# Optimization experiments

Hardware: AMD Instinct MI355X
Metric: run time of the kernel (lower is better)

## Reference

```python
import jax, jax.numpy as jnp
import numpy as np

GRID = 4096
WINDOW_SIZES = (128, 256, 512)  # self.window_schedule in the torch module
BLOCK_FRAC = 0.2                # fraction of blocked (fixed) cells


def setup_inputs() -> dict:
    key = jax.random.key(0)
    u = jax.random.uniform(key, (GRID, GRID), dtype=jnp.float32)
    # blocked cells > 0.0, free cells == 0.0 (binary fixed-cell occupancy mask)
    mask = (u > (1.0 - BLOCK_FRAC)).astype(jnp.float32)
    # the torch code requires the grid center (or an 8-neighbor) to be free;
    # force it free so the seed location is static.
    mask = mask.at[GRID // 2, GRID // 2].set(0.0)
    return {"fixed_cell_mask": mask}


def _dilate4(r):
    # 4-connected dilation of a boolean map (matches BFS neighbor set)
    up = jnp.pad(r[1:, :], ((0, 1), (0, 0)))
    dn = jnp.pad(r[:-1, :], ((1, 0), (0, 0)))
    lf = jnp.pad(r[:, 1:], ((0, 0), (0, 1)))
    rt = jnp.pad(r[:, :-1], ((0, 0), (1, 0)))
    return r | up | dn | lf | rt


def _flood_fill(free, cx, cy):
    """Parallel label-propagation equivalent of the serial BFS flood fill:
    reachable set of `free` cells 4-connected to seed (cx, cy). The seed is
    always tagged, exactly as in get_contiguous_free_region_in_window."""
    seed = jnp.zeros(free.shape, dtype=bool).at[cx, cy].set(True)

    def cond(state):
        reach, prev_count = state
        return jnp.sum(reach) != prev_count

    def body(state):
        reach, _ = state
        new = (_dilate4(reach) & free) | seed
        return new, jnp.sum(reach)

    reach, _ = jax.lax.while_loop(cond, body, (seed, jnp.int32(-1)))
    return reach


def reference(fixed_cell_mask):
    """Faithful JAX version of assemble_free_region_masks: for each window
    size, extract the centered window, flood-fill the contiguous free region
    from the center, and scatter it back into a full-grid boolean mask.
    Returns (masks [len(WINDOW_SIZES), H, W] float32, counts [len] int32)."""
    H, W = fixed_cell_mask.shape
    cx, cy = H // 2, W // 2  # seed is free by construction (see setup_inputs)
    masks, counts = [], []
    for size in WINDOW_SIZES:
        half = size // 2
        sx, ex = max(0, cx - half), min(H, cx + half)
        sy, ey = max(0, cy - half), min(W, cy + half)
        window = fixed_cell_mask[sx:ex, sy:ey]
        free = window == 0.0
        reach = _flood_fill(free, cx - sx, cy - sy)
        full = jnp.zeros((H, W), dtype=bool).at[sx:ex, sy:ey].set(reach)
        masks.append(full)
        counts.append(jnp.sum(reach))
    return jnp.stack(masks).astype(jnp.float32), jnp.stack(counts).astype(jnp.int32)
```

## Files before the change

kernel.cpp:

```cpp
#include <hip/hip_runtime.h>
#include <stdint.h>

#define GRID_N 4096
#define CCL_BLOCKS 336
#define ZERO_BLOCKS 8192
#define K1_BLOCKS (CCL_BLOCKS + ZERO_BLOCKS)
#define CELL_BLOCKS 1344
#define NUM_EDGES 19712
#define EDGE_BLOCKS 77

typedef float vfloat4 __attribute__((ext_vector_type(4)));

__device__ inline void decode_block(int b, int& w, int& S, int& lg, int& off,
                                    int& woff, int& baseblk) {
    if (b < 64)       { w = 0; S = 128; lg = 7; off = 1984; woff = 0;     baseblk = 0;   }
    else if (b < 320) { w = 1; S = 256; lg = 8; off = 1920; woff = 16384; baseblk = 64;  }
    else              { w = 2; S = 512; lg = 9; off = 1792; woff = 81920; baseblk = 320; }
}

__device__ inline void decode_tile(int b, int& S, int& lg, int& off, int& woff,
                                   int& tileR, int& tileC) {
    int t, tsh;
    if (b < 16)      { S = 128; lg = 7; off = 1984; woff = 0;     t = b;      tsh = 2; }
    else if (b < 80) { S = 256; lg = 8; off = 1920; woff = 16384; t = b - 16; tsh = 3; }
    else             { S = 512; lg = 9; off = 1792; woff = 81920; t = b - 80; tsh = 4; }
    tileR = t >> tsh;
    tileC = t & ((1 << tsh) - 1);
}

__device__ inline int uf_find(int* L, int a) {
    while (true) {
        int p = __hip_atomic_load(&L[a], __ATOMIC_RELAXED, __HIP_MEMORY_SCOPE_AGENT);
        if (p == a) return a;
        int gp = __hip_atomic_load(&L[p], __ATOMIC_RELAXED, __HIP_MEMORY_SCOPE_AGENT);
        if (gp == p) return p;
        __hip_atomic_compare_exchange_strong(&L[a], &p, gp,
            __ATOMIC_RELAXED, __ATOMIC_RELAXED, __HIP_MEMORY_SCOPE_AGENT);
        a = gp;
    }
}
__device__ inline void uf_union(int* L, int a, int b) {
    while (true) {
        a = uf_find(L, a);
        b = uf_find(L, b);
        if (a == b) return;
        if (a < b) { int t = a; a = b; b = t; }
        int old = atomicMin(&L[a], b);
        if (old == a) return;
        a = old;
    }
}

__device__ inline int lfind(int* lab, int a) {
    int p = __hip_atomic_load(&lab[a], __ATOMIC_RELAXED, __HIP_MEMORY_SCOPE_WORKGROUP);
    while (p != a) {
        a = p;
        p = __hip_atomic_load(&lab[a], __ATOMIC_RELAXED, __HIP_MEMORY_SCOPE_WORKGROUP);
    }
    return a;
}
__device__ inline void lunion(int* lab, int a, int b) {
    while (true) {
        a = lfind(lab, a);
        b = lfind(lab, b);
        if (a == b) return;
        if (a < b) { int t = a; a = b; b = t; }
        int old = atomicMin(&lab[a], b);
        if (old == a) return;
        a = old;
    }
}

__global__ void k_ccl_zero(const float* __restrict__ mask, int* __restrict__ L,
                           float* __restrict__ out, int out_size) {
    const int b = blockIdx.x;
    if (b < CCL_BLOCKS) {
        int S, lg, off, woff, tileR, tileC;
        decode_tile(b, S, lg, off, woff, tileR, tileC);
        (void)lg;
        __shared__ int lab[1024];

        #pragma unroll
        for (int k = 0; k < 4; k++) {
            int l = threadIdx.x + k * 256;
            int lr = l >> 5, lc = l & 31;
            size_t g = (size_t)(off + tileR * 32 + lr) * GRID_N
                     + (size_t)(off + tileC * 32 + lc);
            lab[l] = (mask[g] == 0.0f) ? l : -1;
        }
        __syncthreads();

        #pragma unroll
        for (int k = 0; k < 4; k++) {
            int l = threadIdx.x + k * 256;
            if (lab[l] == -1) continue;
            int lr = l >> 5, lc = l & 31;
            if (lc + 1 < 32 && lab[l + 1] != -1)  lunion(lab, l, l + 1);
            if (lr + 1 < 32 && lab[l + 32] != -1) lunion(lab, l, l + 32);
        }
        __syncthreads();

        #pragma unroll
        for (int k = 0; k < 4; k++) {
            int l = threadIdx.x + k * 256;
            int lr = l >> 5, lc = l & 31;
            int gidx = (tileR * 32 + lr) * S + tileC * 32 + lc;
            if (lab[l] == -1) {
                L[woff + gidx] = -1;
            } else {
                int r = lfind(lab, l);
                int rr = r >> 5, rc = r & 31;
                L[woff + gidx] = (tileR * 32 + rr) * S + tileC * 32 + rc;
            }
        }
    } else {
        long long n4 = (long long)(out_size >> 2);
        long long i = (long long)(b - CCL_BLOCKS) * 256 + threadIdx.x;
        const long long stride = (long long)ZERO_BLOCKS * 256;
        vfloat4* o4 = (vfloat4*)out;
        vfloat4 z = (vfloat4)(0.0f);
        for (; i < n4; i += stride) o4[i] = z;
        long long t = (long long)(b - CCL_BLOCKS) * 256 + threadIdx.x;
        long long tail = (long long)out_size - n4 * 4;
        if (t < tail) out[n4 * 4 + t] = 0.0f;
    }
}

__global__ void k_edges(int* __restrict__ L) {
    int e = blockIdx.x * 256 + threadIdx.x;
    int S, lg, woff, i; bool vert;
    if (e < 768)        { S = 128; lg = 7; woff = 0;     vert = e < 384;   i = vert ? e : e - 384; }
    else if (e < 4352)  { S = 256; lg = 8; woff = 16384; vert = e < 2560;  i = vert ? e - 768 : e - 2560; }
    else                { S = 512; lg = 9; woff = 81920; vert = e < 12032; i = vert ? e - 4352 : e - 12032; }
    int line = i >> lg;
    int pos = i & (S - 1);
    int* Lw = L + woff;
    int a, n;
    if (vert) { int c = line * 32 + 31; a = pos * S + c; n = a + 1; }
    else      { int r = line * 32 + 31; a = r * S + pos; n = a + S; }
    int la = Lw[a];
    int ln = Lw[n];
    int pla = __shfl_up(la, 1);
    int pln = __shfl_up(ln, 1);
    bool first = ((pos & 31) == 0);
    if (la != -1 && ln != -1 && (first || la != pla || ln != pln))
        uf_union(Lw, la, ln);
}

__global__ void k_write(int* __restrict__ L, float* __restrict__ out) {
    int b = blockIdx.x;
    int w, S, lg, off, woff, baseblk;
    decode_block(b, w, S, lg, off, woff, baseblk);
    int idx = (b - baseblk) * 256 + threadIdx.x;
    int* Lw = L + woff;

    __shared__ int rootC;
    __shared__ float wsum[4];
    if (threadIdx.x == 0) {
        int centerIdx = (S >> 1) * S + (S >> 1);
        rootC = uf_find(Lw, centerIdx);
    }
    __syncthreads();

    int lb = Lw[idx];
    int root = -1;
    unsigned long long need = __ballot(lb != -1);
    while (need) {
        int leader = __builtin_ctzll(need);
        int llab = __shfl(lb, leader);
        int lroot = 0;
        if ((threadIdx.x & 63) == leader) lroot = uf_find(Lw, llab);
        lroot = __shfl(lroot, leader);
        bool match = (lb == llab);
        if (match) root = lroot;
        need &= ~__ballot(match);
    }
    bool reach = (lb != -1) && (root == rootC);

    int r = idx >> lg;
    int c = idx & (S - 1);
    size_t go = (size_t)w * GRID_N * GRID_N + (size_t)(off + r) * GRID_N + (size_t)(off + c);
    out[go] = reach ? 1.0f : 0.0f;

    unsigned long long m = __ballot(reach);
    int lane = threadIdx.x & 63;
    int wv = threadIdx.x >> 6;
    if (lane == 0) wsum[wv] = (float)__popcll(m);
    __syncthreads();
    if (threadIdx.x == 0) {
        float s = wsum[0] + wsum[1] + wsum[2] + wsum[3];
        atomicAdd(&out[(size_t)3 * GRID_N * GRID_N + w], s);
    }
}

extern "C" void kernel_launch(void* const* d_in, const int* in_sizes, int n_in,
                              void* d_out, int out_size, void* d_ws, size_t ws_size,
                              hipStream_t stream) {
    const float* mask = (const float*)d_in[0];
    float* out = (float*)d_out;
    int* L = (int*)d_ws;

    k_ccl_zero<<<K1_BLOCKS, 256, 0, stream>>>(mask, L, out, out_size);
    k_edges<<<EDGE_BLOCKS, 256, 0, stream>>>(L);
    k_write<<<CELL_BLOCKS, 256, 0, stream>>>(L, out);
}
```

Baseline: 265.0 us.

## Split output zero-fill across all three kernels to overlap with CCL phases

The bulk zeroing of the 3×4096×4096 output was done entirely in the first kernel. It is now split into three ranges, each handled by extra blocks appended to one of the three kernels: label-tile, edge-union and write. Range boundaries are chosen so each window's region is zeroed in an earlier launch before the write kernel stores into it, and the count slots are zeroed up front. The goal is to hide the latency-bound edge and write phases behind bandwidth-bound fill work. The risk is that fill blocks compete with the union-find blocks for compute units and delay them.

```diff
diff --git a/kernel.cpp b/kernel.cpp
--- a/kernel.cpp
+++ b/kernel.cpp
@@ -3,11 +3,15 @@
 
 #define GRID_N 4096
 #define CCL_BLOCKS 336
-#define ZERO_BLOCKS 8192
-#define K1_BLOCKS (CCL_BLOCKS + ZERO_BLOCKS)
 #define CELL_BLOCKS 1344
 #define NUM_EDGES 19712
 #define EDGE_BLOCKS 77
+
+#define N4_S1 6422528LL
+#define N4_S2 10747904LL
+#define FILL1_BLOCKS 4096
+#define FILL2_BLOCKS 2048
+#define FILL3_BLOCKS 1024
 
 typedef float vfloat4 __attribute__((ext_vector_type(4)));
 
@@ -71,8 +75,8 @@
     }
 }
 
-__global__ void k_ccl_zero(const float* __restrict__ mask, int* __restrict__ L,
-                           float* __restrict__ out, int out_size) {
+__global__ void k_ccl_fill(const float* __restrict__ mask, int* __restrict__ L,
+                           float* __restrict__ out) {
     const int b = blockIdx.x;
     if (b < CCL_BLOCKS) {
         int S, lg, off, woff, tileR, tileC;
@@ -114,82 +118,99 @@
             }
         }
     } else {
+        long long i = (long long)(b - CCL_BLOCKS) * 256 + threadIdx.x;
+        const long long stride = (long long)FILL1_BLOCKS * 256;
+        vfloat4* o4 = (vfloat4*)out;
+        vfloat4 z = (vfloat4)(0.0f);
+        for (; i < N4_S1; i += stride) o4[i] = z;
+        if (b == CCL_BLOCKS && threadIdx.x < 3)
+            out[(size_t)3 * GRID_N * GRID_N + threadIdx.x] = 0.0f;
+    }
+}
+
+__global__ void k_edges_fill(int* __restrict__ L, float* __restrict__ out) {
+    const int b = blockIdx.x;
+    if (b < EDGE_BLOCKS) {
+        int e = b * 256 + threadIdx.x;
+        int S, lg, woff, i; bool vert;
+        if (e < 768)        { S = 128; lg = 7; woff = 0;     vert = e < 384;   i = vert ? e : e - 384; }
+        else if (e < 4352)  { S = 256; lg = 8; woff = 16384; vert = e < 2560;  i = vert ? e - 768 : e - 2560; }
+        else                { S = 512; lg = 9; woff = 81920; vert = e < 12032; i = vert ? e - 4352 : e - 12032; }
+        int line = i >> lg;
+        int pos = i & (S - 1);
+        int* Lw = L + woff;
+        int a, n;
+        if (vert) { int c = line * 32 + 31; a = pos * S + c; n = a + 1; }
+        else      { int r = line * 32 + 31; a = r * S + pos; n = a + S; }
+        int la = Lw[a];
+        int ln = Lw[n];
+        int pla = __shfl_up(la, 1);
+        int pln = __shfl_up(ln, 1);
+        bool first = ((pos & 31) == 0);
+        if (la != -1 && ln != -1 && (first || la != pla || ln != pln))
+            uf_union(Lw, la, ln);
+    } else {
+        long long i = (long long)(b - EDGE_BLOCKS) * 256 + threadIdx.x + N4_S1;
+        const long long stride = (long long)FILL2_BLOCKS * 256;
+        vfloat4* o4 = (vfloat4*)out;
+        vfloat4 z = (vfloat4)(0.0f);
+        for (; i < N4_S2; i += stride) o4[i] = z;
+    }
+}
+
+__global__ void k_write_fill(int* __restrict__ L, float* __restrict__ out,
+                             int out_size) {
+    const int b = blockIdx.x;
+    if (b < CELL_BLOCKS) {
+        int w, S, lg, off, woff, baseblk;
+        decode_block(b, w, S, lg, off, woff, baseblk);
+        int idx = (b - baseblk) * 256 + threadIdx.x;
+        int* Lw = L + woff;
+
+        __shared__ int rootC;
+        __shared__ float wsum[4];
+        if (threadIdx.x == 0) {
+            int centerIdx = (S >> 1) * S + (S >> 1);
+            rootC = uf_find(Lw, centerIdx);
+        }
+        __syncthreads();
+
+        int lb = Lw[idx];
+        int root = -1;
+        unsigned long long need = __ballot(lb != -1);
+        while (need) {
+            int leader = __builtin_ctzll(need);
+            int llab = __shfl(lb, leader);
+            int lroot = 0;
+            if ((threadIdx.x & 63) == leader) lroot = uf_find(Lw, llab);
+            lroot = __shfl(lroot, leader);
+            bool match = (lb == llab);
+            if (match) root = lroot;
+            need &= ~__ballot(match);
+        }
+        bool reach = (lb != -1) && (root == rootC);
+
+        int r = idx >> lg;
+        int c = idx & (S - 1);
+        size_t go = (size_t)w * GRID_N * GRID_N + (size_t)(off + r) * GRID_N + (size_t)(off + c);
+        out[go] = reach ? 1.0f : 0.0f;
+
+        unsigned long long m = __ballot(reach);
+        int lane = threadIdx.x & 63;
+        int wv = threadIdx.x >> 6;
+        if (lane == 0) wsum[wv] = (float)__popcll(m);
+        __syncthreads();
+        if (threadIdx.x == 0) {
+            float s = wsum[0] + wsum[1] + wsum[2] + wsum[3];
+            atomicAdd(&out[(size_t)3 * GRID_N * GRID_N + w], s);
+        }
+    } else {
         long long n4 = (long long)(out_size >> 2);
-        long long i = (long long)(b - CCL_BLOCKS) * 256 + threadIdx.x;
-        const long long stride = (long long)ZERO_BLOCKS * 256;
+        long long i = (long long)(b - CELL_BLOCKS) * 256 + threadIdx.x + N4_S2;
+        const long long stride = (long long)FILL3_BLOCKS * 256;
         vfloat4* o4 = (vfloat4*)out;
         vfloat4 z = (vfloat4)(0.0f);
         for (; i < n4; i += stride) o4[i] = z;
-        long long t = (long long)(b - CCL_BLOCKS) * 256 + threadIdx.x;
-        long long tail = (long long)out_size - n4 * 4;
-        if (t < tail) out[n4 * 4 + t] = 0.0f;
-    }
-}
-
-__global__ void k_edges(int* __restrict__ L) {
-    int e = blockIdx.x * 256 + threadIdx.x;
-    int S, lg, woff, i; bool vert;
-    if (e < 768)        { S = 128; lg = 7; woff = 0;     vert = e < 384;   i = vert ? e : e - 384; }
-    else if (e < 4352)  { S = 256; lg = 8; woff = 16384; vert = e < 2560;  i = vert ? e - 768 : e - 2560; }
-    else                { S = 512; lg = 9; woff = 81920; vert = e < 12032; i = vert ? e - 4352 : e - 12032; }
-    int line = i >> lg;
-    int pos = i & (S - 1);
-    int* Lw = L + woff;
-    int a, n;
-    if (vert) { int c = line * 32 + 31; a = pos * S + c; n = a + 1; }
-    else      { int r = line * 32 + 31; a = r * S + pos; n = a + S; }
-    int la = Lw[a];
-    int ln = Lw[n];
-    int pla = __shfl_up(la, 1);
-    int pln = __shfl_up(ln, 1);
-    bool first = ((pos & 31) == 0);
-    if (la != -1 && ln != -1 && (first || la != pla || ln != pln))
-        uf_union(Lw, la, ln);
-}
-
-__global__ void k_write(int* __restrict__ L, float* __restrict__ out) {
-    int b = blockIdx.x;
-    int w, S, lg, off, woff, baseblk;
-    decode_block(b, w, S, lg, off, woff, baseblk);
-    int idx = (b - baseblk) * 256 + threadIdx.x;
-    int* Lw = L + woff;
-
-    __shared__ int rootC;
-    __shared__ float wsum[4];
-    if (threadIdx.x == 0) {
-        int centerIdx = (S >> 1) * S + (S >> 1);
-        rootC = uf_find(Lw, centerIdx);
-    }
-    __syncthreads();
-
-    int lb = Lw[idx];
-    int root = -1;
-    unsigned long long need = __ballot(lb != -1);
-    while (need) {
-        int leader = __builtin_ctzll(need);
-        int llab = __shfl(lb, leader);
-        int lroot = 0;
-        if ((threadIdx.x & 63) == leader) lroot = uf_find(Lw, llab);
-        lroot = __shfl(lroot, leader);
-        bool match = (lb == llab);
-        if (match) root = lroot;
-        need &= ~__ballot(match);
-    }
-    bool reach = (lb != -1) && (root == rootC);
-
-    int r = idx >> lg;
-    int c = idx & (S - 1);
-    size_t go = (size_t)w * GRID_N * GRID_N + (size_t)(off + r) * GRID_N + (size_t)(off + c);
-    out[go] = reach ? 1.0f : 0.0f;
-
-    unsigned long long m = __ballot(reach);
-    int lane = threadIdx.x & 63;
-    int wv = threadIdx.x >> 6;
-    if (lane == 0) wsum[wv] = (float)__popcll(m);
-    __syncthreads();
-    if (threadIdx.x == 0) {
-        float s = wsum[0] + wsum[1] + wsum[2] + wsum[3];
-        atomicAdd(&out[(size_t)3 * GRID_N * GRID_N + w], s);
     }
 }
 
@@ -200,7 +221,7 @@
     float* out = (float*)d_out;
     int* L = (int*)d_ws;
 
-    k_ccl_zero<<<K1_BLOCKS, 256, 0, stream>>>(mask, L, out, out_size);
-    k_edges<<<EDGE_BLOCKS, 256, 0, stream>>>(L);
-    k_write<<<CELL_BLOCKS, 256, 0, stream>>>(L, out);
-}
+    k_ccl_fill<<<CCL_BLOCKS + FILL1_BLOCKS, 256, 0, stream>>>(mask, L, out);
+    k_edges_fill<<<EDGE_BLOCKS + FILL2_BLOCKS, 256, 0, stream>>>(L, out);
+    k_write_fill<<<CELL_BLOCKS + FILL3_BLOCKS, 256, 0, stream>>>(L, out, out_size);
+}
```

New measurement: 263.8 us. Within noise of the previous version (-0.5%).
